# Kernel optimization log

Hardware: AMD Instinct MI355X
Metric: run time of the kernel (lower is better)

## Reference

```python
import jax, jax.numpy as jnp
import numpy as np

INPUT_SIZE = 512
HIDDEN_SIZE = 512


def setup_inputs() -> dict:
    key = jax.random.key(0)
    k1, k2, k3, k4, k5 = jax.random.split(key, 5)
    B, N = 8, 2048
    x = jax.random.normal(k1, (B, N, INPUT_SIZE), dtype=jnp.float32)
    # Linear params (torch nn.Linear: y = x @ W^T + b), init scale ~ 1/sqrt(fan_in)
    s = 1.0 / np.sqrt(INPUT_SIZE)
    Wq = jax.random.uniform(k2, (HIDDEN_SIZE, INPUT_SIZE), minval=-s, maxval=s, dtype=jnp.float32)
    bq = jax.random.uniform(k3, (HIDDEN_SIZE,), minval=-s, maxval=s, dtype=jnp.float32)
    Wk = jax.random.uniform(k4, (HIDDEN_SIZE, INPUT_SIZE), minval=-s, maxval=s, dtype=jnp.float32)
    bk = jax.random.uniform(k5, (HIDDEN_SIZE,), minval=-s, maxval=s, dtype=jnp.float32)
    return {"x": x, "Wq": Wq, "bq": bq, "Wk": Wk, "bk": bk}


def reference(x, Wq, bq, Wk, bk):
    # q, k: [B, N, H]
    q = jnp.einsum('bnd,hd->bnh', x, Wq) + bq
    k = jnp.einsum('bnd,hd->bnh', x, Wk) + bk
    # scores: [B, N, N], softmax over last axis (dim=2)
    scores = jnp.einsum('bnh,bmh->bnm', q, k) / jnp.sqrt(jnp.float32(HIDDEN_SIZE))
    attn = jax.nn.softmax(scores, axis=2)
    # attended = attn^T @ x : [B, N, input_size]; squeeze(2) no-op since input_size>1
    attended = jnp.einsum('bnm,bnd->bmd', attn, x)
    return attended
```

## Files before the change

### kernel.cpp

```cpp
#include <hip/hip_runtime.h>

typedef __bf16 bf16x8 __attribute__((ext_vector_type(8)));
typedef __bf16 bf16x4 __attribute__((ext_vector_type(4)));
typedef float f32x4 __attribute__((ext_vector_type(4)));

__device__ __forceinline__ void async_copy16(const void* g, void* l) {
    __builtin_amdgcn_global_load_lds(
        (const __attribute__((address_space(1))) void*)g,
        (__attribute__((address_space(3))) void*)l, 16, 0, 0);
}

__device__ __forceinline__ int xcd_swz(int bx, int nx) {
    return (bx & 7) * (nx >> 3) + (bx >> 3);
}

__global__ __launch_bounds__(256) void k_cvt(
    const float4* __restrict__ x, const float4* __restrict__ Wq,
    const float4* __restrict__ Wk, const float4* __restrict__ bq,
    const float4* __restrict__ bk,
    bf16x4* __restrict__ xb, bf16x4* __restrict__ Wb,
    float4* __restrict__ biasc) {
    int i = blockIdx.x * 256 + threadIdx.x;
    if (i < 2097152) {
        float4 v = x[i];
        bf16x4 r = {(__bf16)v.x, (__bf16)v.y, (__bf16)v.z, (__bf16)v.w};
        xb[i] = r;
    }
    if (i < 131072) {
        float4 v = (i < 65536) ? Wq[i] : Wk[i - 65536];
        bf16x4 r = {(__bf16)v.x, (__bf16)v.y, (__bf16)v.z, (__bf16)v.w};
        Wb[i] = r;
    }
    if (i < 256) {
        biasc[i] = (i < 128) ? bq[i] : bk[i - 128];
    }
}

__global__ __launch_bounds__(256) void k_fold(
    const __bf16* __restrict__ xb, const float* __restrict__ Z,
    ushort* __restrict__ xzT) {
    __shared__ float tile[64][65];
    __shared__ float zin[64];
    const int b = blockIdx.y;
    const int td = blockIdx.x & 7;
    const int tn = blockIdx.x >> 3;
    const int n0 = tn * 64, d0 = td * 64;
    const int t = threadIdx.x;
    if (t < 64) zin[t] = 1.0f / Z[b * 2048 + n0 + t];
    __syncthreads();
    const int cl = t & 15, c4 = cl * 4, rr = t >> 4;
#pragma unroll
    for (int j = 0; j < 4; ++j) {
        int nr = rr + j * 16;
        bf16x4 v = *(const bf16x4*)&xb[((size_t)b * 2048 + n0 + nr) * 512 + d0 + c4];
        tile[nr][c4 + 0] = (float)v[0];
        tile[nr][c4 + 1] = (float)v[1];
        tile[nr][c4 + 2] = (float)v[2];
        tile[nr][c4 + 3] = (float)v[3];
    }
    __syncthreads();
#pragma unroll
    for (int j2 = 0; j2 < 4; ++j2) {
        int dr = rr + j2 * 16;
        bf16x4 pk;
#pragma unroll
        for (int j = 0; j < 4; ++j)
            pk[j] = (__bf16)(tile[j * 16 + cl][dr] * zin[c4 + j]);
        *(bf16x4*)&xzT[((size_t)b * 512 + d0 + dr) * 2048 + n0 + c4] = pk;
    }
}

template <int EPI>
__device__ __forceinline__ void gemm_core(
    const ushort* __restrict__ A, int lda, long sA,
    const ushort* __restrict__ B, int ldb, long sB,
    void* __restrict__ C, int ldc, long sC,
    int tiles_n, int K,
    const float* __restrict__ bias, float scale2,
    float* __restrict__ Z, long sZ) {
    __shared__ ushort lA[2][8192];
    __shared__ ushort lB[2][8192];
    const int b = blockIdx.y;
    A += (size_t)b * sA;
    B += (size_t)b * sB;
    const int bx = xcd_swz(blockIdx.x, gridDim.x);
    const int tm = bx / tiles_n, tn = bx % tiles_n;
    const int t = threadIdx.x;
    const int l = t & 63, w = t >> 6;
    const int wr = w >> 1, wc = w & 1;

    size_t gA[4], gB[4];
    int dOf[4];
#pragma unroll
    for (int p = 0; p < 4; ++p) {
        int off = p * 4096 + t * 16;
        int row = off >> 7, kb = off & 127;
        int kswz = kb ^ ((row & 7) << 4);
        gA[p] = (size_t)(tm * 128 + row) * lda + (kswz >> 1);
        gB[p] = (size_t)(tn * 128 + row) * ldb + (kswz >> 1);
        dOf[p] = off;
    }
    auto stage = [&](int buf, int k0) {
#pragma unroll
        for (int p = 0; p < 4; ++p) {
            async_copy16(A + gA[p] + k0, (char*)lA[buf] + dOf[p]);
            async_copy16(B + gB[p] + k0, (char*)lB[buf] + dOf[p]);
        }
    };

    f32x4 acc[4][4];
#pragma unroll
    for (int i = 0; i < 4; ++i)
#pragma unroll
        for (int j = 0; j < 4; ++j) acc[i][j] = (f32x4){0.f, 0.f, 0.f, 0.f};

    const int nk = K >> 6;
    stage(0, 0);
    stage(1, 64);
    asm volatile("s_waitcnt vmcnt(8)" ::: "memory");
    __builtin_amdgcn_s_barrier();
    asm volatile("" ::: "memory");

    for (int kt = 0; kt < nk; ++kt) {
        const int cur = kt & 1;
        bf16x8 af[4][2], bg[4][2];
#pragma unroll
        for (int ks = 0; ks < 2; ++ks)
#pragma unroll
            for (int i = 0; i < 4; ++i) {
                int rowA = wr * 64 + i * 16 + (l & 15);
                int colA = (ks * 64 + (l >> 4) * 16) ^ ((rowA & 7) << 4);
                af[i][ks] = *(const bf16x8*)((const char*)lA[cur] + rowA * 128 + colA);
                int rowB = wc * 64 + i * 16 + (l & 15);
                int colB = (ks * 64 + (l >> 4) * 16) ^ ((rowB & 7) << 4);
                bg[i][ks] = *(const bf16x8*)((const char*)lB[cur] + rowB * 128 + colB);
            }
        asm volatile("s_waitcnt lgkmcnt(0)" ::: "memory");
        __builtin_amdgcn_sched_barrier(0);
        __builtin_amdgcn_s_barrier();
        asm volatile("" ::: "memory");
        if (kt + 2 < nk) stage(cur, (kt + 2) << 6);
        __builtin_amdgcn_sched_barrier(0);
        __builtin_amdgcn_s_setprio(1);
#pragma unroll
        for (int ks = 0; ks < 2; ++ks)
#pragma unroll
            for (int i = 0; i < 4; ++i)
#pragma unroll
                for (int j = 0; j < 4; ++j)
                    acc[i][j] = __builtin_amdgcn_mfma_f32_16x16x32_bf16(
                        af[i][ks], bg[j][ks], acc[i][j], 0, 0, 0);
        __builtin_amdgcn_s_setprio(0);
        if (kt + 2 < nk) {
            asm volatile("s_waitcnt vmcnt(8)" ::: "memory");
        } else {
            asm volatile("s_waitcnt vmcnt(0)" ::: "memory");
        }
        __builtin_amdgcn_s_barrier();
        asm volatile("" ::: "memory");
    }

    const int mb = tm * 128 + wr * 64;
    const int nb = tn * 128 + wc * 64;
    const int cl = l & 15;

    if (EPI == 0) {
        ushort* Cp = (ushort*)C + (size_t)b * sC;
#pragma unroll
        for (int i = 0; i < 4; ++i)
#pragma unroll
            for (int q = 0; q < 4; ++q) {
                int row = mb + i * 16 + (l >> 4) * 4 + q;
                bf16x4 pk;
#pragma unroll
                for (int j = 0; j < 4; ++j)
                    pk[j] = (__bf16)(acc[i][j][q] + bias[nb + j * 16 + cl]);
                *(bf16x4*)&Cp[(size_t)row * ldc + nb + cl * 4] = pk;
            }
    } else if (EPI == 1) {
        ushort* Cp = (ushort*)C + (size_t)b * sC;
        float colsum[4] = {0.f, 0.f, 0.f, 0.f};
#pragma unroll
        for (int i = 0; i < 4; ++i)
#pragma unroll
            for (int q = 0; q < 4; ++q) {
                int row = mb + i * 16 + (l >> 4) * 4 + q;
                bf16x4 pk;
#pragma unroll
                for (int j = 0; j < 4; ++j) {
                    float e = __builtin_amdgcn_exp2f(acc[i][j][q] * scale2);
                    colsum[j] += e;
                    pk[j] = (__bf16)e;
                }
                *(bf16x4*)&Cp[(size_t)row * ldc + nb + cl * 4] = pk;
            }
#pragma unroll
        for (int j = 0; j < 4; ++j) {
            float s = colsum[j];
            s += __shfl_xor(s, 16);
            s += __shfl_xor(s, 32);
            if (l < 16) atomicAdd(&Z[b * sZ + nb + l * 4 + j], s);
        }
    } else {
        float* Cp = (float*)C + (size_t)b * sC;
#pragma unroll
        for (int i = 0; i < 4; ++i)
#pragma unroll
            for (int j = 0; j < 4; ++j)
#pragma unroll
                for (int q = 0; q < 4; ++q) {
                    int row = mb + i * 16 + (l >> 4) * 4 + q;
                    int col = nb + j * 16 + cl;
                    Cp[(size_t)row * ldc + col] = acc[i][j][q];
                }
    }
}

__global__ __launch_bounds__(256) void k_proj(
    const ushort* __restrict__ A, const ushort* __restrict__ B,
    ushort* __restrict__ C, const float* __restrict__ bias) {
    gemm_core<0>(A, 512, 0L, B, 512, 0L, C, 1024, 0L,
                 8, 512, bias, 0.f, nullptr, 0L);
}

__global__ __launch_bounds__(256) void k_escore(
    const ushort* __restrict__ A, const ushort* __restrict__ B,
    ushort* __restrict__ C, float* __restrict__ Z) {
    gemm_core<1>(A, 1024, 2048L * 1024, B, 1024, 2048L * 1024,
                 C, 2048, 2048L * 2048, 16, 512,
                 nullptr, 0.063758716f, Z, 2048L);
}

__global__ __launch_bounds__(256) void k_out(
    const ushort* __restrict__ A, const ushort* __restrict__ B,
    float* __restrict__ C) {
    gemm_core<2>(A, 2048, 2048L * 2048, B, 2048, 512L * 2048,
                 C, 512, 2048L * 512, 4, 2048,
                 nullptr, 0.f, nullptr, 0L);
}

extern "C" void kernel_launch(void* const* d_in, const int* in_sizes, int n_in,
                              void* d_out, int out_size, void* d_ws, size_t ws_size,
                              hipStream_t stream) {
    const float* x  = (const float*)d_in[0];
    const float* Wq = (const float*)d_in[1];
    const float* bq = (const float*)d_in[2];
    const float* Wk = (const float*)d_in[3];
    const float* bk = (const float*)d_in[4];

    char* ws = (char*)d_ws;
    ushort* xb    = (ushort*)(ws);
    ushort* Wb    = (ushort*)(ws + 16777216);
    float*  biasc = (float*) (ws + 17825792);
    float*  Z     = (float*) (ws + 17829888);
    ushort* qkb   = (ushort*)(ws + 17895424);
    ushort* E     = (ushort*)(ws + 51449856);
    ushort* xzT   = qkb;

    (void)hipMemsetAsync(Z, 0, 16384 * 4, stream);

    k_cvt<<<8192, 256, 0, stream>>>(
        (const float4*)x, (const float4*)Wq, (const float4*)Wk,
        (const float4*)bq, (const float4*)bk,
        (bf16x4*)xb, (bf16x4*)Wb, (float4*)biasc);

    k_proj<<<dim3(1024, 1), 256, 0, stream>>>(xb, Wb, qkb, biasc);

    k_escore<<<dim3(256, 8), 256, 0, stream>>>(qkb + 512, qkb, E, Z);

    k_fold<<<dim3(256, 8), 256, 0, stream>>>((const __bf16*)xb, Z, xzT);

    k_out<<<dim3(64, 8), 256, 0, stream>>>(E, xzT, (float*)d_out);
}
```

Baseline: 132.6 us.

## Use 256x256 tile 8-wave pipelined GEMM for projection and score kernels

Replaces the 128x128, 4-wave GEMM used by the projection and exp-score kernels with a new 256x256 tile, 512-thread kernel that uses 128KB of dynamic LDS. It keeps a four-slot async copy pipeline whose stages are interleaved with half-tile MFMA phases, so more data is reused per loaded byte and copies overlap compute. The output GEMM keeps the old kernel, now inlined. Risks are fewer blocks per grid (wave quantization on 256 CUs), high register pressure from 32 accumulators per wave, and needing the dynamic shared memory attribute set at static init.

```diff
diff --git a/kernel.cpp b/kernel.cpp
--- a/kernel.cpp
+++ b/kernel.cpp
@@ -31,9 +31,7 @@
         bf16x4 r = {(__bf16)v.x, (__bf16)v.y, (__bf16)v.z, (__bf16)v.w};
         Wb[i] = r;
     }
-    if (i < 256) {
-        biasc[i] = (i < 128) ? bq[i] : bk[i - 128];
-    }
+    if (i < 256) biasc[i] = (i < 128) ? bq[i] : bk[i - 128];
 }
 
 __global__ __launch_bounds__(256) void k_fold(
@@ -71,18 +69,193 @@
 }
 
 template <int EPI>
-__device__ __forceinline__ void gemm_core(
+__device__ __forceinline__ void gemm8p(
     const ushort* __restrict__ A, int lda, long sA,
     const ushort* __restrict__ B, int ldb, long sB,
-    void* __restrict__ C, int ldc, long sC,
+    ushort* __restrict__ C, int ldc, long sC,
     int tiles_n, int K,
     const float* __restrict__ bias, float scale2,
     float* __restrict__ Z, long sZ) {
-    __shared__ ushort lA[2][8192];
-    __shared__ ushort lB[2][8192];
+    extern __shared__ char lds[];
     const int b = blockIdx.y;
     A += (size_t)b * sA;
     B += (size_t)b * sB;
+    const int bx = xcd_swz(blockIdx.x, gridDim.x);
+    const int tm = bx / tiles_n, tn = bx % tiles_n;
+    const int t = threadIdx.x;
+    const int l = t & 63, w = t >> 6;
+    const int wr = w >> 2, wc = w & 3;
+    const int l15 = l & 15, g16 = l >> 4;
+
+    size_t gAo[2], gBo[2];
+    int dst[2];
+#pragma unroll
+    for (int p = 0; p < 2; ++p) {
+        int off = p * 8192 + t * 16;
+        int P = off >> 7, sl = (off >> 4) & 7;
+        int u = sl ^ (P & 7);
+        int rg = 2 * P + (u >> 2);
+        int kb8 = (u & 3) * 8;
+        gAo[p] = (size_t)(tm * 256 + rg) * lda + kb8;
+        gBo[p] = (size_t)(tn * 256 + rg) * ldb + kb8;
+        dst[p] = off;
+    }
+
+#define REG_A(d, ks) (((d) * 2 + (ks)) * 16384)
+#define REG_B(d, ks) (65536 + ((d) * 2 + (ks)) * 16384)
+#define STG_A(d, ks, kk)                                              \
+    { int ro = REG_A(d, ks);                                          \
+      async_copy16(A + gAo[0] + (kk), lds + ro + dst[0]);             \
+      async_copy16(A + gAo[1] + (kk), lds + ro + dst[1]); }
+#define STG_B(d, ks, kk)                                              \
+    { int ro = REG_B(d, ks);                                          \
+      async_copy16(B + gBo[0] + (kk), lds + ro + dst[0]);             \
+      async_copy16(B + gBo[1] + (kk), lds + ro + dst[1]); }
+
+    auto rdoff = [&](int row) {
+        int P = row >> 1;
+        int slot = (((row & 1) << 2) | g16) ^ (P & 7);
+        return P * 128 + slot * 16;
+    };
+
+    f32x4 acc[8][4];
+#pragma unroll
+    for (int i = 0; i < 8; ++i)
+#pragma unroll
+        for (int j = 0; j < 4; ++j) acc[i][j] = (f32x4){0.f, 0.f, 0.f, 0.f};
+
+    bf16x8 af[4], bg[4];
+
+#define RD_B(d, ks)                                                   \
+    _Pragma("unroll") for (int j = 0; j < 4; ++j)                     \
+        bg[j] = *(const bf16x8*)(lds + REG_B(d, ks) +                 \
+                                 rdoff(wc * 64 + j * 16 + l15));
+#define RD_A(d, ks, isub)                                             \
+    _Pragma("unroll") for (int i = 0; i < 4; ++i)                     \
+        af[i] = *(const bf16x8*)(lds + REG_A(d, ks) +                 \
+                                 rdoff(wr * 128 + (isub) * 64 + i * 16 + l15));
+#define DO_MFMA(isub)                                                 \
+    __builtin_amdgcn_s_setprio(1);                                    \
+    _Pragma("unroll") for (int i = 0; i < 4; ++i)                     \
+        _Pragma("unroll") for (int j = 0; j < 4; ++j)                 \
+            acc[(isub) * 4 + i][j] = __builtin_amdgcn_mfma_f32_16x16x32_bf16( \
+                af[i], bg[j], acc[(isub) * 4 + i][j], 0, 0, 0);       \
+    __builtin_amdgcn_s_setprio(0);
+#define SYNC_LGKM                                                     \
+    asm volatile("s_waitcnt lgkmcnt(0)" ::: "memory");                \
+    __builtin_amdgcn_sched_barrier(0);
+#define ENDPH(vm)                                                     \
+    if (vm) asm volatile("s_waitcnt vmcnt(4)" ::: "memory");          \
+    __builtin_amdgcn_s_barrier();                                     \
+    asm volatile("" ::: "memory");                                    \
+    __builtin_amdgcn_sched_barrier(0);
+
+    STG_B(0, 0, 0); STG_A(0, 0, 0);
+    STG_B(0, 1, 32); STG_A(0, 1, 32);
+    STG_B(1, 0, 64); STG_A(1, 0, 64);
+    asm volatile("s_waitcnt vmcnt(4)" ::: "memory");
+    __builtin_amdgcn_s_barrier();
+    asm volatile("" ::: "memory");
+
+    const int NI = K >> 7;
+    for (int it = 0; it < NI; ++it) {
+        const int kb = it << 7;
+        const int kn = (it + 1 < NI) ? (kb + 128) : kb;
+        RD_B(0, 0); RD_A(0, 0, 0); STG_B(1, 1, kb + 96);
+        SYNC_LGKM; DO_MFMA(0); ENDPH(false);
+        RD_A(0, 0, 1); STG_A(1, 1, kb + 96);
+        SYNC_LGKM; DO_MFMA(1); ENDPH(false);
+        RD_B(0, 1); RD_A(0, 1, 0); STG_B(0, 0, kn);
+        SYNC_LGKM; DO_MFMA(0); ENDPH(false);
+        RD_A(0, 1, 1); STG_A(0, 0, kn);
+        SYNC_LGKM; DO_MFMA(1); ENDPH(true);
+        RD_B(1, 0); RD_A(1, 0, 0); STG_B(0, 1, kn + 32);
+        SYNC_LGKM; DO_MFMA(0); ENDPH(false);
+        RD_A(1, 0, 1); STG_A(0, 1, kn + 32);
+        SYNC_LGKM; DO_MFMA(1); ENDPH(false);
+        RD_B(1, 1); RD_A(1, 1, 0); STG_B(1, 0, kn + 64);
+        SYNC_LGKM; DO_MFMA(0); ENDPH(false);
+        RD_A(1, 1, 1); STG_A(1, 0, kn + 64);
+        SYNC_LGKM; DO_MFMA(1); ENDPH(true);
+    }
+    asm volatile("s_waitcnt vmcnt(0)" ::: "memory");
+
+    const int mb = tm * 256 + wr * 128;
+    const int nb = tn * 256 + wc * 64;
+    const int cl = l15;
+    ushort* Cp = C + (size_t)b * sC;
+
+    if (EPI == 0) {
+#pragma unroll
+        for (int i = 0; i < 8; ++i)
+#pragma unroll
+            for (int q = 0; q < 4; ++q) {
+                int row = mb + i * 16 + (l >> 4) * 4 + q;
+                bf16x4 pk;
+#pragma unroll
+                for (int j = 0; j < 4; ++j)
+                    pk[j] = (__bf16)(acc[i][j][q] + bias[nb + j * 16 + cl]);
+                *(bf16x4*)&Cp[(size_t)row * ldc + nb + cl * 4] = pk;
+            }
+    } else {
+        float colsum[4] = {0.f, 0.f, 0.f, 0.f};
+#pragma unroll
+        for (int i = 0; i < 8; ++i)
+#pragma unroll
+            for (int q = 0; q < 4; ++q) {
+                int row = mb + i * 16 + (l >> 4) * 4 + q;
+                bf16x4 pk;
+#pragma unroll
+                for (int j = 0; j < 4; ++j) {
+                    float e = __builtin_amdgcn_exp2f(acc[i][j][q] * scale2);
+                    colsum[j] += e;
+                    pk[j] = (__bf16)e;
+                }
+                *(bf16x4*)&Cp[(size_t)row * ldc + nb + cl * 4] = pk;
+            }
+#pragma unroll
+        for (int j = 0; j < 4; ++j) {
+            float s = colsum[j];
+            s += __shfl_xor(s, 16);
+            s += __shfl_xor(s, 32);
+            if (l < 16) atomicAdd(&Z[b * sZ + nb + l * 4 + j], s);
+        }
+    }
+#undef REG_A
+#undef REG_B
+#undef STG_A
+#undef STG_B
+#undef RD_A
+#undef RD_B
+#undef DO_MFMA
+#undef SYNC_LGKM
+#undef ENDPH
+}
+
+__global__ __launch_bounds__(512, 2) void k_proj8(
+    const ushort* __restrict__ A, const ushort* __restrict__ B,
+    ushort* __restrict__ C, const float* __restrict__ bias) {
+    gemm8p<0>(A, 512, 0L, B, 512, 0L, C, 1024, 0L,
+              4, 512, bias, 0.f, nullptr, 0L);
+}
+
+__global__ __launch_bounds__(512, 2) void k_escore8(
+    const ushort* __restrict__ A, const ushort* __restrict__ B,
+    ushort* __restrict__ C, float* __restrict__ Z) {
+    gemm8p<1>(A, 1024, 2048L * 1024, B, 1024, 2048L * 1024,
+              C, 2048, 2048L * 2048, 8, 512,
+              nullptr, 0.063758716f, Z, 2048L);
+}
+
+__global__ __launch_bounds__(256) void k_out(
+    const ushort* __restrict__ Ain, const ushort* __restrict__ Bin,
+    float* __restrict__ Cout) {
+    __shared__ ushort lA[2][8192];
+    __shared__ ushort lB[2][8192];
+    const int lda = 2048, ldb = 2048, ldc = 512, tiles_n = 4, K = 2048;
+    const int b = blockIdx.y;
+    const ushort* A = Ain + (size_t)b * 2048L * 2048;
+    const ushort* B = Bin + (size_t)b * 512L * 2048;
     const int bx = xcd_swz(blockIdx.x, gridDim.x);
     const int tm = bx / tiles_n, tn = bx % tiles_n;
     const int t = threadIdx.x;
@@ -162,81 +335,29 @@
 
     const int mb = tm * 128 + wr * 64;
     const int nb = tn * 128 + wc * 64;
-    const int cl = l & 15;
-
-    if (EPI == 0) {
-        ushort* Cp = (ushort*)C + (size_t)b * sC;
-#pragma unroll
-        for (int i = 0; i < 4; ++i)
+    float* Cp = Cout + (size_t)b * 2048L * 512;
+#pragma unroll
+    for (int i = 0; i < 4; ++i)
+#pragma unroll
+        for (int j = 0; j < 4; ++j)
 #pragma unroll
             for (int q = 0; q < 4; ++q) {
                 int row = mb + i * 16 + (l >> 4) * 4 + q;
-                bf16x4 pk;
-#pragma unroll
-                for (int j = 0; j < 4; ++j)
-                    pk[j] = (__bf16)(acc[i][j][q] + bias[nb + j * 16 + cl]);
-                *(bf16x4*)&Cp[(size_t)row * ldc + nb + cl * 4] = pk;
+                int col = nb + j * 16 + (l & 15);
+                Cp[(size_t)row * ldc + col] = acc[i][j][q];
             }
-    } else if (EPI == 1) {
-        ushort* Cp = (ushort*)C + (size_t)b * sC;
-        float colsum[4] = {0.f, 0.f, 0.f, 0.f};
-#pragma unroll
-        for (int i = 0; i < 4; ++i)
-#pragma unroll
-            for (int q = 0; q < 4; ++q) {
-                int row = mb + i * 16 + (l >> 4) * 4 + q;
-                bf16x4 pk;
-#pragma unroll
-                for (int j = 0; j < 4; ++j) {
-                    float e = __builtin_amdgcn_exp2f(acc[i][j][q] * scale2);
-                    colsum[j] += e;
-                    pk[j] = (__bf16)e;
-                }
-                *(bf16x4*)&Cp[(size_t)row * ldc + nb + cl * 4] = pk;
-            }
-#pragma unroll
-        for (int j = 0; j < 4; ++j) {
-            float s = colsum[j];
-            s += __shfl_xor(s, 16);
-            s += __shfl_xor(s, 32);
-            if (l < 16) atomicAdd(&Z[b * sZ + nb + l * 4 + j], s);
-        }
-    } else {
-        float* Cp = (float*)C + (size_t)b * sC;
-#pragma unroll
-        for (int i = 0; i < 4; ++i)
-#pragma unroll
-            for (int j = 0; j < 4; ++j)
-#pragma unroll
-                for (int q = 0; q < 4; ++q) {
-                    int row = mb + i * 16 + (l >> 4) * 4 + q;
-                    int col = nb + j * 16 + cl;
-                    Cp[(size_t)row * ldc + col] = acc[i][j][q];
-                }
-    }
-}
-
-__global__ __launch_bounds__(256) void k_proj(
-    const ushort* __restrict__ A, const ushort* __restrict__ B,
-    ushort* __restrict__ C, const float* __restrict__ bias) {
-    gemm_core<0>(A, 512, 0L, B, 512, 0L, C, 1024, 0L,
-                 8, 512, bias, 0.f, nullptr, 0L);
-}
-
-__global__ __launch_bounds__(256) void k_escore(
-    const ushort* __restrict__ A, const ushort* __restrict__ B,
-    ushort* __restrict__ C, float* __restrict__ Z) {
-    gemm_core<1>(A, 1024, 2048L * 1024, B, 1024, 2048L * 1024,
-                 C, 2048, 2048L * 2048, 16, 512,
-                 nullptr, 0.063758716f, Z, 2048L);
-}
-
-__global__ __launch_bounds__(256) void k_out(
-    const ushort* __restrict__ A, const ushort* __restrict__ B,
-    float* __restrict__ C) {
-    gemm_core<2>(A, 2048, 2048L * 2048, B, 2048, 512L * 2048,
-                 C, 512, 2048L * 512, 4, 2048,
-                 nullptr, 0.f, nullptr, 0L);
+}
+
+namespace {
+struct AttrInit {
+    AttrInit() {
+        hipFuncSetAttribute(reinterpret_cast<const void*>(&k_proj8),
+                            hipFuncAttributeMaxDynamicSharedMemorySize, 131072);
+        hipFuncSetAttribute(reinterpret_cast<const void*>(&k_escore8),
+                            hipFuncAttributeMaxDynamicSharedMemorySize, 131072);
+    }
+};
+AttrInit attr_init_;
 }
 
 extern "C" void kernel_launch(void* const* d_in, const int* in_sizes, int n_in,
@@ -264,9 +385,9 @@
         (const float4*)bq, (const float4*)bk,
         (bf16x4*)xb, (bf16x4*)Wb, (float4*)biasc);
 
-    k_proj<<<dim3(1024, 1), 256, 0, stream>>>(xb, Wb, qkb, biasc);
-
-    k_escore<<<dim3(256, 8), 256, 0, stream>>>(qkb + 512, qkb, E, Z);
+    k_proj8<<<dim3(256, 1), 512, 131072, stream>>>(xb, Wb, qkb, biasc);
+
+    k_escore8<<<dim3(64, 8), 512, 131072, stream>>>(qkb + 512, qkb, E, Z);
 
     k_fold<<<dim3(256, 8), 256, 0, stream>>>((const __bf16*)xb, Z, xzT);
 
```

New measurement: 127.5 us. -3.9%, faster.
